# Kernel optimization log

Hardware: AMD Instinct MI355X
Metric: run time of the kernel (lower is better)

Reference implementation:

```python
import jax, jax.numpy as jnp
import numpy as np

N_NODES = 100000


def _sage_conv(x, edge_index, W_l, b_l, W_r):
    # PyG SAGEConv (aggr='mean', root_weight=True, normalize=False):
    # out = lin_l(mean_{j in N(i)} x_j) + lin_r(x_i)
    src, dst = edge_index[0], edge_index[1]
    n = x.shape[0]
    agg = jax.ops.segment_sum(x[src], dst, num_segments=n)
    cnt = jax.ops.segment_sum(jnp.ones((src.shape[0],), x.dtype), dst, num_segments=n)
    agg = agg / jnp.maximum(cnt, 1.0)[:, None]
    return agg @ W_l + b_l + x @ W_r


def setup_inputs() -> dict:
    key = jax.random.key(0)
    ks = jax.random.split(key, 12)
    in_dim, hidden = 384, 128
    x = jax.random.normal(ks[0], (N_NODES, in_dim), dtype=jnp.float32)
    edge_index = jax.random.randint(ks[1], (2, 3200000), 0, N_NODES, dtype=jnp.int32)
    pos_edge_label_index = jax.random.randint(ks[2], (2, 500000), 0, N_NODES, dtype=jnp.int32)
    neg_edge_label_index = jax.random.randint(ks[3], (2, 500000), 0, N_NODES, dtype=jnp.int32)
    s1 = 1.0 / np.sqrt(in_dim)
    s2 = 1.0 / np.sqrt(hidden)
    return {
        "x": x,
        "edge_index": edge_index,
        "pos_edge_label_index": pos_edge_label_index,
        "neg_edge_label_index": neg_edge_label_index,
        "W_l1": jax.random.uniform(ks[4], (in_dim, hidden), jnp.float32, -s1, s1),
        "b_l1": jnp.zeros((hidden,), jnp.float32),
        "W_r1": jax.random.uniform(ks[5], (in_dim, hidden), jnp.float32, -s1, s1),
        "W_l2": jax.random.uniform(ks[6], (hidden, hidden), jnp.float32, -s2, s2),
        "b_l2": jnp.zeros((hidden,), jnp.float32),
        "W_r2": jax.random.uniform(ks[7], (hidden, hidden), jnp.float32, -s2, s2),
        "W_lin": jax.random.uniform(ks[8], (2 * hidden, 1), jnp.float32, -s2, s2),
        "b_lin": jnp.zeros((1,), jnp.float32),
    }


def reference(x, edge_index, pos_edge_label_index, neg_edge_label_index,
              W_l1, b_l1, W_r1, W_l2, b_l2, W_r2, W_lin, b_lin):
    h = _sage_conv(x, edge_index, W_l1, b_l1, W_r1)
    h = jax.nn.relu(h)
    h = _sage_conv(h, edge_index, W_l2, b_l2, W_r2)

    def score(idx):
        pair = jnp.concatenate([h[idx[0]], h[idx[1]]], axis=1)  # [E, 2*hidden]
        return (pair @ W_lin + b_lin).reshape(-1)

    return score(pos_edge_label_index), score(neg_edge_label_index)
```

## Files before the change

### kernel.cpp

```cpp
#include <hip/hip_runtime.h>

#define IN_DIM 384
#define HID    128
#define NPB    256
#define BCAP   16384
#define LCAP   10240

#define AS1 __attribute__((address_space(1)))
#define AS3 __attribute__((address_space(3)))

typedef _Float16 half8 __attribute__((ext_vector_type(8)));
typedef _Float16 half2t __attribute__((ext_vector_type(2)));
typedef __fp16 fp16x2 __attribute__((ext_vector_type(2)));
typedef float floatx4 __attribute__((ext_vector_type(4)));

__global__ void zero_i32(int* __restrict__ p, int n) {
  int i = blockIdx.x * 256 + threadIdx.x;
  if (i < n) p[i] = 0;
}

__global__ __launch_bounds__(512) void partition_kernel(
    const int* __restrict__ src, const int* __restrict__ dst, int E, int nB,
    int* __restrict__ bCur, unsigned* __restrict__ bucketData) {
  __shared__ int hist[391];
  __shared__ int gbase[391];
  const int t = threadIdx.x;
  const int b0 = blockIdx.x * 8192;

  for (int i = t; i < nB; i += 512) hist[i] = 0;
  __syncthreads();
#pragma unroll
  for (int i = 0; i < 16; ++i) {
    int e = b0 + i * 512 + t;
    if (e < E) atomicAdd(&hist[dst[e] >> 8], 1);
  }
  __syncthreads();
  for (int i = t; i < nB; i += 512) {
    int h = hist[i];
    gbase[i] = h ? (i * BCAP + atomicAdd(&bCur[i], h)) : 0;
    hist[i] = 0;
  }
  __syncthreads();
#pragma unroll
  for (int i = 0; i < 16; ++i) {
    int e = b0 + i * 512 + t;
    if (e < E) {
      int d = dst[e];
      int b = d >> 8;
      int r = atomicAdd(&hist[b], 1);
      bucketData[gbase[b] + r] = ((unsigned)(d & 255) << 17) | (unsigned)src[e];
    }
  }
}

__global__ __launch_bounds__(1024) void node_sort3(
    const unsigned* __restrict__ bucketData, const int* __restrict__ bCur,
    int N, int* __restrict__ sorted_src, int* __restrict__ rs, int* __restrict__ re) {
  extern __shared__ unsigned sdata[];
  __shared__ int hist[NPB];
  __shared__ int s[NPB];
  __shared__ int cur[NPB];
  const int b = blockIdx.x;
  const int t = threadIdx.x;
  const int start = b * BCAP;
  const int fill = bCur[b];
  if (t < NPB) hist[t] = 0;
  __syncthreads();
  for (int i = t; i < fill; i += 1024) {
    unsigned d = bucketData[start + i];
    if (i < LCAP) sdata[i] = d;
    atomicAdd(&hist[d >> 17], 1);
  }
  __syncthreads();
  int v = 0;
  if (t < NPB) { v = hist[t]; s[t] = v; }
  __syncthreads();
  for (int off = 1; off < NPB; off <<= 1) {
    int y = (t < NPB && t >= off) ? s[t - off] : 0;
    __syncthreads();
    if (t < NPB) s[t] += y;
    __syncthreads();
  }
  if (t < NPB) {
    int excl = s[t] - v;
    const int node = b * NPB + t;
    if (node < N) {
      rs[node] = start + excl;
      re[node] = start + excl + v;
    }
    cur[t] = start + excl;
  }
  __syncthreads();
  for (int i = t; i < fill; i += 1024) {
    unsigned d = (i < LCAP) ? sdata[i] : bucketData[start + i];
    int p = atomicAdd(&cur[d >> 17], 1);
    sorted_src[p] = (int)(d & 0x1FFFF);
  }
}

__global__ void pack_w2(const float* __restrict__ Wl, const float* __restrict__ Wr,
                        _Float16* __restrict__ Bp) {
  const float* __restrict__ W = blockIdx.z ? Wr : Wl;
  const int tn = blockIdx.x;
  const int ks = blockIdx.y;
  const int KS = gridDim.y;
  const int lane = threadIdx.x;
  const int n = tn * 16 + (lane & 15);
  const int kb = ks * 32 + (lane >> 4) * 8;
  half8 v;
#pragma unroll
  for (int j = 0; j < 8; ++j) v[j] = (_Float16)W[(size_t)(kb + j) * HID + n];
  *(half8*)(Bp + (((size_t)(blockIdx.z * 8 + tn) * KS + ks) * 64 + lane) * 8) = v;
}

__device__ inline half2t cvt_pk(float a, float b) {
  fp16x2 r = __builtin_amdgcn_cvt_pkrtz(a, b);
  union { fp16x2 f; half2t h; } c;
  c.f = r;
  return c.h;
}

__global__ __launch_bounds__(512) void gemm_f32a(
    const float* __restrict__ A, int M,
    const _Float16* __restrict__ Bp, _Float16* __restrict__ C) {
  __shared__ float As[128 * 32];

  const int K = IN_DIM, KS = IN_DIM / 32;
  const int tid = threadIdx.x;
  const int lane = tid & 63;
  const int wid = tid >> 6;
  const int quad = lane >> 4;
  const int lm = lane & 15;
  const int row0 = (wid & 1) * 64;
  const int ct0 = (wid >> 1) * 4;
  const int blockRow = blockIdx.x * 128;

  const int srow = lane >> 3;
  const int scol = ((lane & 7) ^ (srow & 7)) * 4;
  const int grow0 = min(blockRow + wid * 16 + srow, M - 1);
  const int grow1 = min(blockRow + wid * 16 + 8 + srow, M - 1);

  floatx4 acc[16];
#pragma unroll
  for (int i = 0; i < 16; ++i) {
    acc[i][0] = 0.f; acc[i][1] = 0.f; acc[i][2] = 0.f; acc[i][3] = 0.f;
  }

  for (int ks = 0; ks < KS; ++ks) {
    const int k0 = ks * 32;
    __syncthreads();
    __builtin_amdgcn_global_load_lds(
        (const AS1 void*)(A + (size_t)grow0 * K + k0 + scol),
        (AS3 void*)(As + (wid * 16) * 32), 16, 0, 0);
    __builtin_amdgcn_global_load_lds(
        (const AS1 void*)(A + (size_t)grow1 * K + k0 + scol),
        (AS3 void*)(As + (wid * 16 + 8) * 32), 16, 0, 0);

    half8 bf[4];
#pragma unroll
    for (int ct = 0; ct < 4; ++ct)
      bf[ct] = *(const half8*)(Bp + (((size_t)(ct0 + ct) * KS + ks) * 64 + lane) * 8);

    __syncthreads();

    half8 af[4];
#pragma unroll
    for (int rt = 0; rt < 4; ++rt) {
      const int row = row0 + rt * 16 + lm;
      const int sw = row & 7;
      const floatx4 fA = *(const floatx4*)&As[(row * 8 + ((quad * 2) ^ sw)) * 4];
      const floatx4 fB = *(const floatx4*)&As[(row * 8 + ((quad * 2 + 1) ^ sw)) * 4];
      half2t h01 = cvt_pk(fA[0], fA[1]);
      half2t h23 = cvt_pk(fA[2], fA[3]);
      half2t h45 = cvt_pk(fB[0], fB[1]);
      half2t h67 = cvt_pk(fB[2], fB[3]);
      half8 a;
      a[0] = h01[0]; a[1] = h01[1]; a[2] = h23[0]; a[3] = h23[1];
      a[4] = h45[0]; a[5] = h45[1]; a[6] = h67[0]; a[7] = h67[1];
      af[rt] = a;
    }
#pragma unroll
    for (int rt = 0; rt < 4; ++rt)
#pragma unroll
      for (int ct = 0; ct < 4; ++ct)
        acc[rt * 4 + ct] =
            __builtin_amdgcn_mfma_f32_16x16x32_f16(af[rt], bf[ct], acc[rt * 4 + ct], 0, 0, 0);
  }

#pragma unroll
  for (int rt = 0; rt < 4; ++rt) {
#pragma unroll
    for (int r = 0; r < 4; ++r) {
      const int gm = blockRow + row0 + rt * 16 + quad * 4 + r;
      if (gm < M) {
#pragma unroll
        for (int ct = 0; ct < 4; ++ct)
          C[(size_t)gm * 256 + (ct0 + ct) * 16 + lm] = (_Float16)acc[rt * 4 + ct][r];
      }
    }
  }
}

__global__ __launch_bounds__(512) void gemm_f16a(
    const _Float16* __restrict__ A, int M,
    const _Float16* __restrict__ Bp, _Float16* __restrict__ C) {
  __shared__ _Float16 As[128 * 32];

  const int K = HID, KS = HID / 32;
  const int tid = threadIdx.x;
  const int lane = tid & 63;
  const int wid = tid >> 6;
  const int quad = lane >> 4;
  const int lm = lane & 15;
  const int row0 = (wid & 1) * 64;
  const int ct0 = (wid >> 1) * 4;
  const int blockRow = blockIdx.x * 128;

  const int srow = lane >> 2;
  const int scol = ((lane & 3) ^ ((lane >> 3) & 3)) * 8;
  const int grow = min(blockRow + wid * 16 + srow, M - 1);

  floatx4 acc[16];
#pragma unroll
  for (int i = 0; i < 16; ++i) {
    acc[i][0] = 0.f; acc[i][1] = 0.f; acc[i][2] = 0.f; acc[i][3] = 0.f;
  }

  for (int ks = 0; ks < KS; ++ks) {
    const int k0 = ks * 32;
    __syncthreads();
    __builtin_amdgcn_global_load_lds(
        (const AS1 void*)(A + (size_t)grow * K + k0 + scol),
        (AS3 void*)(As + (wid * 16) * 32), 16, 0, 0);

    half8 bf[4];
#pragma unroll
    for (int ct = 0; ct < 4; ++ct)
      bf[ct] = *(const half8*)(Bp + (((size_t)(ct0 + ct) * KS + ks) * 64 + lane) * 8);

    __syncthreads();

    half8 af[4];
#pragma unroll
    for (int rt = 0; rt < 4; ++rt) {
      const int row = row0 + rt * 16 + lm;
      const int cg = quad ^ ((row >> 1) & 3);
      af[rt] = *(const half8*)&As[(row * 4 + cg) * 8];
    }
#pragma unroll
    for (int rt = 0; rt < 4; ++rt)
#pragma unroll
      for (int ct = 0; ct < 4; ++ct)
        acc[rt * 4 + ct] =
            __builtin_amdgcn_mfma_f32_16x16x32_f16(af[rt], bf[ct], acc[rt * 4 + ct], 0, 0, 0);
  }

#pragma unroll
  for (int rt = 0; rt < 4; ++rt) {
#pragma unroll
    for (int r = 0; r < 4; ++r) {
      const int gm = blockRow + row0 + rt * 16 + quad * 4 + r;
      if (gm < M) {
#pragma unroll
        for (int ct = 0; ct < 4; ++ct)
          C[(size_t)gm * 256 + (ct0 + ct) * 16 + lm] = (_Float16)acc[rt * 4 + ct][r];
      }
    }
  }
}

__device__ inline float2 upk(unsigned u) {
  union { unsigned v; _Float16 h[2]; } c; c.v = u;
  return make_float2((float)c.h[0], (float)c.h[1]);
}
__device__ inline half2t as_h2(unsigned u) {
  union { unsigned v; half2t h; } c; c.v = u;
  return c.h;
}
__device__ inline unsigned as_u32(half2t h) {
  union { half2t h; unsigned v; } c; c.h = h;
  return c.v;
}
__device__ inline unsigned pkadd(unsigned a, unsigned b) {
  return as_u32(as_h2(a) + as_h2(b));
}
__device__ inline void pkacc4(uint4& A, const uint4& v) {
  A.x = pkadd(A.x, v.x); A.y = pkadd(A.y, v.y);
  A.z = pkadd(A.z, v.z); A.w = pkadd(A.w, v.w);
}

__device__ inline uint4 gather_rows(const unsigned* __restrict__ yzu,
                                    const int* __restrict__ sorted_src,
                                    int start, int end, int cl, int slot) {
  uint4 A0 = make_uint4(0u, 0u, 0u, 0u);
  uint4 A1 = A0;
  int k = start + slot;
  for (; k + 12 < end; k += 16) {
    int s0 = sorted_src[k];
    int s1 = sorted_src[k + 4];
    int s2 = sorted_src[k + 8];
    int s3 = sorted_src[k + 12];
    uint4 v0 = *(const uint4*)(yzu + (size_t)s0 * 128 + cl * 4);
    uint4 v1 = *(const uint4*)(yzu + (size_t)s1 * 128 + cl * 4);
    uint4 v2 = *(const uint4*)(yzu + (size_t)s2 * 128 + cl * 4);
    uint4 v3 = *(const uint4*)(yzu + (size_t)s3 * 128 + cl * 4);
    pkacc4(A0, v0);
    pkacc4(A1, v1);
    pkacc4(A0, v2);
    pkacc4(A1, v3);
  }
  if (k + 4 < end) {
    int s0 = sorted_src[k];
    int s1 = sorted_src[k + 4];
    uint4 v0 = *(const uint4*)(yzu + (size_t)s0 * 128 + cl * 4);
    uint4 v1 = *(const uint4*)(yzu + (size_t)s1 * 128 + cl * 4);
    pkacc4(A0, v0);
    pkacc4(A1, v1);
    k += 8;
  }
  if (k < end) {
    int s = sorted_src[k];
    uint4 v = *(const uint4*)(yzu + (size_t)s * 128 + cl * 4);
    pkacc4(A0, v);
  }
  pkacc4(A0, A1);
#pragma unroll
  for (int off = 16; off < 64; off <<= 1) {
    uint4 o;
    o.x = (unsigned)__shfl_xor((int)A0.x, off, 64);
    o.y = (unsigned)__shfl_xor((int)A0.y, off, 64);
    o.z = (unsigned)__shfl_xor((int)A0.z, off, 64);
    o.w = (unsigned)__shfl_xor((int)A0.w, off, 64);
    pkacc4(A0, o);
  }
  return A0;
}

__global__ __launch_bounds__(256) void agg_relu16(
    const unsigned* __restrict__ yzu, const int* __restrict__ sorted_src,
    const int* __restrict__ rs, const int* __restrict__ re,
    const float* __restrict__ bias, unsigned* __restrict__ h1u, int N) {
  const int w = threadIdx.x >> 6;
  const int lane = threadIdx.x & 63;
  const int cl = lane & 15;
  const int slot = lane >> 4;
  const int node = blockIdx.x * 4 + w;
  if (node >= N) return;
  const int start = rs[node];
  const int end = re[node];
  uint4 A = gather_rows(yzu, sorted_src, start, end, cl, slot);
  if (slot == 0) {
    const int deg = end - start;
    const float inv = 1.f / (float)max(deg, 1);
    uint4 z4 = *(const uint4*)(yzu + (size_t)node * 128 + 64 + cl * 4);
    const unsigned av[4] = {A.x, A.y, A.z, A.w};
    const unsigned zv[4] = {z4.x, z4.y, z4.z, z4.w};
    uint4 o;
    unsigned ov[4];
#pragma unroll
    for (int q = 0; q < 4; ++q) {
      const int cp = cl * 4 + q;
      float2 a = upk(av[q]);
      float2 z = upk(zv[q]);
      float vx = fmaxf(a.x * inv + bias[2 * cp] + z.x, 0.f);
      float vy = fmaxf(a.y * inv + bias[2 * cp + 1] + z.y, 0.f);
      union { unsigned v; _Float16 h[2]; } c;
      c.h[0] = (_Float16)vx; c.h[1] = (_Float16)vy;
      ov[q] = c.v;
    }
    o.x = ov[0]; o.y = ov[1]; o.z = ov[2]; o.w = ov[3];
    *(uint4*)(h1u + (size_t)node * 64 + cl * 4) = o;
  }
}

__global__ __launch_bounds__(256) void agg_score16(
    const unsigned* __restrict__ yzu, const int* __restrict__ sorted_src,
    const int* __restrict__ rs, const int* __restrict__ re,
    const float* __restrict__ bias, const float* __restrict__ Wlin,
    float* __restrict__ sa, float* __restrict__ sb, int N) {
  const int w = threadIdx.x >> 6;
  const int lane = threadIdx.x & 63;
  const int cl = lane & 15;
  const int slot = lane >> 4;
  const int node = blockIdx.x * 4 + w;
  if (node >= N) return;
  const int start = rs[node];
  const int end = re[node];
  uint4 A = gather_rows(yzu, sorted_src, start, end, cl, slot);
  const int deg = end - start;
  const float inv = 1.f / (float)max(deg, 1);
  uint4 z4 = *(const uint4*)(yzu + (size_t)node * 128 + 64 + cl * 4);
  const unsigned av[4] = {A.x, A.y, A.z, A.w};
  const unsigned zv[4] = {z4.x, z4.y, z4.z, z4.w};
  float pa = 0.f, pb = 0.f;
#pragma unroll
  for (int q = 0; q < 4; ++q) {
    const int cp = cl * 4 + q;
    float2 a = upk(av[q]);
    float2 z = upk(zv[q]);
    float hx = a.x * inv + bias[2 * cp] + z.x;
    float hy = a.y * inv + bias[2 * cp + 1] + z.y;
    pa += hx * Wlin[2 * cp] + hy * Wlin[2 * cp + 1];
    pb += hx * Wlin[128 + 2 * cp] + hy * Wlin[129 + 2 * cp];
  }
#pragma unroll
  for (int off = 1; off < 16; off <<= 1) {
    pa += __shfl_xor(pa, off, 64);
    pb += __shfl_xor(pb, off, 64);
  }
  if (lane == 0) {
    sa[node] = pa;
    sb[node] = pb;
  }
}

__global__ void score2(const int* __restrict__ pos, const int* __restrict__ neg,
                       int Ep, int En,
                       const float* __restrict__ sa, const float* __restrict__ sb,
                       const float* __restrict__ blin, float* __restrict__ out) {
  int e = blockIdx.x * 256 + threadIdx.x;
  if (e < Ep) {
    out[e] = sa[pos[e]] + sb[pos[Ep + e]] + blin[0];
  } else if (e < Ep + En) {
    int i = e - Ep;
    out[Ep + i] = sa[neg[i]] + sb[neg[En + i]] + blin[0];
  }
}

extern "C" void kernel_launch(void* const* d_in, const int* in_sizes, int n_in,
                              void* d_out, int out_size, void* d_ws, size_t ws_size,
                              hipStream_t stream) {
  (void)n_in; (void)out_size; (void)ws_size;
  const float* x    = (const float*)d_in[0];
  const int*   ei   = (const int*)d_in[1];
  const int*   pos  = (const int*)d_in[2];
  const int*   neg  = (const int*)d_in[3];
  const float* Wl1  = (const float*)d_in[4];
  const float* bl1  = (const float*)d_in[5];
  const float* Wr1  = (const float*)d_in[6];
  const float* Wl2  = (const float*)d_in[7];
  const float* bl2  = (const float*)d_in[8];
  const float* Wr2  = (const float*)d_in[9];
  const float* Wlin = (const float*)d_in[10];
  const float* blin = (const float*)d_in[11];

  const int N  = in_sizes[0] / IN_DIM;
  const int E  = in_sizes[1] / 2;
  const int Ep = in_sizes[2] / 2;
  const int En = in_sizes[3] / 2;
  const int* e_src = ei;
  const int* e_dst = ei + E;

  char* ws = (char*)d_ws;
  size_t off = 0;
  auto carve = [&](size_t bytes) -> char* {
    char* p = ws + off;
    off += (bytes + 255) & ~(size_t)255;
    return p;
  };
  const int nB = (N + NPB - 1) / NPB;
  const int KS1 = IN_DIM / 32;
  const int KS2 = HID / 32;

  int*      rs     = (int*)carve((size_t)N * 4);
  int*      re     = (int*)carve((size_t)N * 4);
  int*      bCur   = (int*)carve(512 * 4);
  unsigned* bData  = (unsigned*)carve((size_t)nB * BCAP * 4);
  int*      sorted = (int*)carve((size_t)nB * BCAP * 4);
  float*    sa     = (float*)carve((size_t)N * 4);
  float*    sb     = (float*)carve((size_t)N * 4);
  _Float16* Bp1    = (_Float16*)carve((size_t)16 * KS1 * 64 * 8 * 2);
  _Float16* Bp2    = (_Float16*)carve((size_t)16 * KS2 * 64 * 8 * 2);
  _Float16* yz     = (_Float16*)carve((size_t)N * 256 * 2);
  _Float16* h1     = (_Float16*)carve((size_t)N * 128 * 2);

  const int gemmBlocks = (N + 127) / 128;
  const int partBlocks = (E + 8191) / 8192;

  hipLaunchKernelGGL(zero_i32, dim3(2), dim3(256), 0, stream, bCur, 512);
  hipLaunchKernelGGL(partition_kernel, dim3(partBlocks), dim3(512), 0, stream,
                     e_src, e_dst, E, nB, bCur, bData);
  hipLaunchKernelGGL(node_sort3, dim3(nB), dim3(1024), LCAP * 4, stream,
                     bData, bCur, N, sorted, rs, re);

  hipLaunchKernelGGL(pack_w2, dim3(8, KS1, 2), dim3(64), 0, stream, Wl1, Wr1, Bp1);
  hipLaunchKernelGGL(pack_w2, dim3(8, KS2, 2), dim3(64), 0, stream, Wl2, Wr2, Bp2);

  hipLaunchKernelGGL(gemm_f32a, dim3(gemmBlocks), dim3(512), 0, stream,
                     x, N, Bp1, yz);
  hipLaunchKernelGGL(agg_relu16, dim3((N + 3) / 4), dim3(256), 0, stream,
                     (const unsigned*)yz, sorted, rs, re, bl1, (unsigned*)h1, N);
  hipLaunchKernelGGL(gemm_f16a, dim3(gemmBlocks), dim3(512), 0, stream,
                     h1, N, Bp2, yz);
  hipLaunchKernelGGL(agg_score16, dim3((N + 3) / 4), dim3(256), 0, stream,
                     (const unsigned*)yz, sorted, rs, re, bl2, Wlin, sa, sb, N);

  float* out = (float*)d_out;
  hipLaunchKernelGGL(score2, dim3((Ep + En + 255) / 256), dim3(256), 0, stream,
                     pos, neg, Ep, En, sa, sb, blin, out);
}
```

Before: 593.1 us.

## Split GEMM output into column-group planes and aggregate per group for cache locality

The GEMM outputs are now written in a column-group-major layout: eight planes of 16 half columns for the neighbour projection and eight for the root projection. The aggregation kernels launch eight times as many blocks, and each block gathers only its 32-byte slice per neighbour, so the table each block touches is small enough to stay cache-resident. The score kernel now accumulates partial dot products with float atomics, and the partition kernel zeroes the sa/sb buffers first. The cost is eight reads of each index list, many more atomics, strided GEMM stores, and 32-byte gathers that may use memory transactions poorly.

```diff
diff --git a/kernel.cpp b/kernel.cpp
--- a/kernel.cpp
+++ b/kernel.cpp
@@ -21,11 +21,14 @@
 
 __global__ __launch_bounds__(512) void partition_kernel(
     const int* __restrict__ src, const int* __restrict__ dst, int E, int nB,
-    int* __restrict__ bCur, unsigned* __restrict__ bucketData) {
+    int* __restrict__ bCur, unsigned* __restrict__ bucketData,
+    float* __restrict__ sab, int sabN) {
   __shared__ int hist[391];
   __shared__ int gbase[391];
   const int t = threadIdx.x;
   const int b0 = blockIdx.x * 8192;
+
+  for (int i = blockIdx.x * 512 + t; i < sabN; i += gridDim.x * 512) sab[i] = 0.f;
 
   for (int i = t; i < nB; i += 512) hist[i] = 0;
   __syncthreads();
@@ -119,6 +122,7 @@
   c.f = r;
   return c.h;
 }
+
 
 __global__ __launch_bounds__(512) void gemm_f32a(
     const float* __restrict__ A, int M,
@@ -194,8 +198,12 @@
       const int gm = blockRow + row0 + rt * 16 + quad * 4 + r;
       if (gm < M) {
 #pragma unroll
-        for (int ct = 0; ct < 4; ++ct)
-          C[(size_t)gm * 256 + (ct0 + ct) * 16 + lm] = (_Float16)acc[rt * 4 + ct][r];
+        for (int ct = 0; ct < 4; ++ct) {
+          const int tn = ct0 + ct;
+          _Float16* dst = C + ((size_t)(tn & 7) * M + gm) * 16 + lm;
+          if (tn >= 8) dst += (size_t)M * 128;
+          *dst = (_Float16)acc[rt * 4 + ct][r];
+        }
       }
     }
   }
@@ -262,8 +270,12 @@
       const int gm = blockRow + row0 + rt * 16 + quad * 4 + r;
       if (gm < M) {
 #pragma unroll
-        for (int ct = 0; ct < 4; ++ct)
-          C[(size_t)gm * 256 + (ct0 + ct) * 16 + lm] = (_Float16)acc[rt * 4 + ct][r];
+        for (int ct = 0; ct < 4; ++ct) {
+          const int tn = ct0 + ct;
+          _Float16* dst = C + ((size_t)(tn & 7) * M + gm) * 16 + lm;
+          if (tn >= 8) dst += (size_t)M * 128;
+          *dst = (_Float16)acc[rt * 4 + ct][r];
+        }
       }
     }
   }
@@ -284,133 +296,115 @@
 __device__ inline unsigned pkadd(unsigned a, unsigned b) {
   return as_u32(as_h2(a) + as_h2(b));
 }
-__device__ inline void pkacc4(uint4& A, const uint4& v) {
-  A.x = pkadd(A.x, v.x); A.y = pkadd(A.y, v.y);
-  A.z = pkadd(A.z, v.z); A.w = pkadd(A.w, v.w);
-}
-
-__device__ inline uint4 gather_rows(const unsigned* __restrict__ yzu,
-                                    const int* __restrict__ sorted_src,
-                                    int start, int end, int cl, int slot) {
-  uint4 A0 = make_uint4(0u, 0u, 0u, 0u);
-  uint4 A1 = A0;
+__device__ inline uint2 pkadd2(uint2 a, uint2 b) {
+  a.x = pkadd(a.x, b.x); a.y = pkadd(a.y, b.y); return a;
+}
+
+__device__ inline uint2 gather_group(const unsigned* __restrict__ yg,
+                                     const int* __restrict__ sorted_src,
+                                     int start, int end, int cl, int slot) {
+  uint2 A0 = make_uint2(0u, 0u);
+  uint2 A1 = make_uint2(0u, 0u);
   int k = start + slot;
-  for (; k + 12 < end; k += 16) {
+  for (; k + 16 < end; k += 32) {
     int s0 = sorted_src[k];
-    int s1 = sorted_src[k + 4];
-    int s2 = sorted_src[k + 8];
-    int s3 = sorted_src[k + 12];
-    uint4 v0 = *(const uint4*)(yzu + (size_t)s0 * 128 + cl * 4);
-    uint4 v1 = *(const uint4*)(yzu + (size_t)s1 * 128 + cl * 4);
-    uint4 v2 = *(const uint4*)(yzu + (size_t)s2 * 128 + cl * 4);
-    uint4 v3 = *(const uint4*)(yzu + (size_t)s3 * 128 + cl * 4);
-    pkacc4(A0, v0);
-    pkacc4(A1, v1);
-    pkacc4(A0, v2);
-    pkacc4(A1, v3);
-  }
-  if (k + 4 < end) {
-    int s0 = sorted_src[k];
-    int s1 = sorted_src[k + 4];
-    uint4 v0 = *(const uint4*)(yzu + (size_t)s0 * 128 + cl * 4);
-    uint4 v1 = *(const uint4*)(yzu + (size_t)s1 * 128 + cl * 4);
-    pkacc4(A0, v0);
-    pkacc4(A1, v1);
-    k += 8;
+    int s1 = sorted_src[k + 16];
+    uint2 v0 = *(const uint2*)(yg + (size_t)s0 * 8 + cl * 2);
+    uint2 v1 = *(const uint2*)(yg + (size_t)s1 * 8 + cl * 2);
+    A0 = pkadd2(A0, v0);
+    A1 = pkadd2(A1, v1);
   }
   if (k < end) {
-    int s = sorted_src[k];
-    uint4 v = *(const uint4*)(yzu + (size_t)s * 128 + cl * 4);
-    pkacc4(A0, v);
-  }
-  pkacc4(A0, A1);
-#pragma unroll
-  for (int off = 16; off < 64; off <<= 1) {
-    uint4 o;
+    uint2 v = *(const uint2*)(yg + (size_t)sorted_src[k] * 8 + cl * 2);
+    A0 = pkadd2(A0, v);
+  }
+  A0 = pkadd2(A0, A1);
+#pragma unroll
+  for (int off = 4; off < 64; off <<= 1) {
+    uint2 o;
     o.x = (unsigned)__shfl_xor((int)A0.x, off, 64);
     o.y = (unsigned)__shfl_xor((int)A0.y, off, 64);
-    o.z = (unsigned)__shfl_xor((int)A0.z, off, 64);
-    o.w = (unsigned)__shfl_xor((int)A0.w, off, 64);
-    pkacc4(A0, o);
+    A0 = pkadd2(A0, o);
   }
   return A0;
 }
 
-__global__ __launch_bounds__(256) void agg_relu16(
+__global__ __launch_bounds__(256) void agg_relu_split(
     const unsigned* __restrict__ yzu, const int* __restrict__ sorted_src,
     const int* __restrict__ rs, const int* __restrict__ re,
     const float* __restrict__ bias, unsigned* __restrict__ h1u, int N) {
+  const int g = blockIdx.x & 7;
+  const int nb = blockIdx.x >> 3;
   const int w = threadIdx.x >> 6;
   const int lane = threadIdx.x & 63;
-  const int cl = lane & 15;
-  const int slot = lane >> 4;
-  const int node = blockIdx.x * 4 + w;
+  const int cl = lane & 3;
+  const int slot = lane >> 2;
+  const int node = nb * 4 + w;
   if (node >= N) return;
   const int start = rs[node];
   const int end = re[node];
-  uint4 A = gather_rows(yzu, sorted_src, start, end, cl, slot);
+  const unsigned* __restrict__ yg = yzu + (size_t)g * N * 8;
+  uint2 A = gather_group(yg, sorted_src, start, end, cl, slot);
   if (slot == 0) {
     const int deg = end - start;
     const float inv = 1.f / (float)max(deg, 1);
-    uint4 z4 = *(const uint4*)(yzu + (size_t)node * 128 + 64 + cl * 4);
-    const unsigned av[4] = {A.x, A.y, A.z, A.w};
-    const unsigned zv[4] = {z4.x, z4.y, z4.z, z4.w};
-    uint4 o;
-    unsigned ov[4];
-#pragma unroll
-    for (int q = 0; q < 4; ++q) {
-      const int cp = cl * 4 + q;
-      float2 a = upk(av[q]);
-      float2 z = upk(zv[q]);
-      float vx = fmaxf(a.x * inv + bias[2 * cp] + z.x, 0.f);
-      float vy = fmaxf(a.y * inv + bias[2 * cp + 1] + z.y, 0.f);
-      union { unsigned v; _Float16 h[2]; } c;
-      c.h[0] = (_Float16)vx; c.h[1] = (_Float16)vy;
-      ov[q] = c.v;
-    }
-    o.x = ov[0]; o.y = ov[1]; o.z = ov[2]; o.w = ov[3];
-    *(uint4*)(h1u + (size_t)node * 64 + cl * 4) = o;
-  }
-}
-
-__global__ __launch_bounds__(256) void agg_score16(
+    uint2 z2 = *(const uint2*)(yzu + (size_t)N * 64 + ((size_t)g * N + node) * 8 + cl * 2);
+    float2 a0 = upk(A.x);
+    float2 a1 = upk(A.y);
+    float2 z0 = upk(z2.x);
+    float2 z1 = upk(z2.y);
+    const int c = g * 16 + cl * 4;
+    float v0 = fmaxf(a0.x * inv + bias[c]     + z0.x, 0.f);
+    float v1 = fmaxf(a0.y * inv + bias[c + 1] + z0.y, 0.f);
+    float v2 = fmaxf(a1.x * inv + bias[c + 2] + z1.x, 0.f);
+    float v3 = fmaxf(a1.y * inv + bias[c + 3] + z1.y, 0.f);
+    union { unsigned v; _Float16 h[2]; } cc;
+    uint2 o;
+    cc.h[0] = (_Float16)v0; cc.h[1] = (_Float16)v1; o.x = cc.v;
+    cc.h[0] = (_Float16)v2; cc.h[1] = (_Float16)v3; o.y = cc.v;
+    *(uint2*)(h1u + (size_t)node * 64 + g * 8 + cl * 2) = o;
+  }
+}
+
+__global__ __launch_bounds__(256) void agg_score_split(
     const unsigned* __restrict__ yzu, const int* __restrict__ sorted_src,
     const int* __restrict__ rs, const int* __restrict__ re,
     const float* __restrict__ bias, const float* __restrict__ Wlin,
     float* __restrict__ sa, float* __restrict__ sb, int N) {
+  const int g = blockIdx.x & 7;
+  const int nb = blockIdx.x >> 3;
   const int w = threadIdx.x >> 6;
   const int lane = threadIdx.x & 63;
-  const int cl = lane & 15;
-  const int slot = lane >> 4;
-  const int node = blockIdx.x * 4 + w;
+  const int cl = lane & 3;
+  const int slot = lane >> 2;
+  const int node = nb * 4 + w;
   if (node >= N) return;
   const int start = rs[node];
   const int end = re[node];
-  uint4 A = gather_rows(yzu, sorted_src, start, end, cl, slot);
-  const int deg = end - start;
-  const float inv = 1.f / (float)max(deg, 1);
-  uint4 z4 = *(const uint4*)(yzu + (size_t)node * 128 + 64 + cl * 4);
-  const unsigned av[4] = {A.x, A.y, A.z, A.w};
-  const unsigned zv[4] = {z4.x, z4.y, z4.z, z4.w};
-  float pa = 0.f, pb = 0.f;
-#pragma unroll
-  for (int q = 0; q < 4; ++q) {
-    const int cp = cl * 4 + q;
-    float2 a = upk(av[q]);
-    float2 z = upk(zv[q]);
-    float hx = a.x * inv + bias[2 * cp] + z.x;
-    float hy = a.y * inv + bias[2 * cp + 1] + z.y;
-    pa += hx * Wlin[2 * cp] + hy * Wlin[2 * cp + 1];
-    pb += hx * Wlin[128 + 2 * cp] + hy * Wlin[129 + 2 * cp];
-  }
-#pragma unroll
-  for (int off = 1; off < 16; off <<= 1) {
-    pa += __shfl_xor(pa, off, 64);
-    pb += __shfl_xor(pb, off, 64);
-  }
-  if (lane == 0) {
-    sa[node] = pa;
-    sb[node] = pb;
+  const unsigned* __restrict__ yg = yzu + (size_t)g * N * 8;
+  uint2 A = gather_group(yg, sorted_src, start, end, cl, slot);
+  if (slot == 0) {
+    const int deg = end - start;
+    const float inv = 1.f / (float)max(deg, 1);
+    uint2 z2 = *(const uint2*)(yzu + (size_t)N * 64 + ((size_t)g * N + node) * 8 + cl * 2);
+    float2 a0 = upk(A.x);
+    float2 a1 = upk(A.y);
+    float2 z0 = upk(z2.x);
+    float2 z1 = upk(z2.y);
+    const int c = g * 16 + cl * 4;
+    float h0 = a0.x * inv + bias[c]     + z0.x;
+    float h1 = a0.y * inv + bias[c + 1] + z0.y;
+    float h2 = a1.x * inv + bias[c + 2] + z1.x;
+    float h3 = a1.y * inv + bias[c + 3] + z1.y;
+    float pa = h0 * Wlin[c] + h1 * Wlin[c + 1] + h2 * Wlin[c + 2] + h3 * Wlin[c + 3];
+    float pb = h0 * Wlin[128 + c] + h1 * Wlin[129 + c] +
+               h2 * Wlin[130 + c] + h3 * Wlin[131 + c];
+    pa += __shfl_xor(pa, 1, 64); pb += __shfl_xor(pb, 1, 64);
+    pa += __shfl_xor(pa, 2, 64); pb += __shfl_xor(pb, 2, 64);
+    if (cl == 0) {
+      atomicAdd(&sa[node], pa);
+      atomicAdd(&sb[node], pb);
+    }
   }
 }
 
@@ -467,19 +461,22 @@
   int*      bCur   = (int*)carve(512 * 4);
   unsigned* bData  = (unsigned*)carve((size_t)nB * BCAP * 4);
   int*      sorted = (int*)carve((size_t)nB * BCAP * 4);
-  float*    sa     = (float*)carve((size_t)N * 4);
-  float*    sb     = (float*)carve((size_t)N * 4);
+  float*    sab    = (float*)carve((size_t)2 * N * 4);
   _Float16* Bp1    = (_Float16*)carve((size_t)16 * KS1 * 64 * 8 * 2);
   _Float16* Bp2    = (_Float16*)carve((size_t)16 * KS2 * 64 * 8 * 2);
   _Float16* yz     = (_Float16*)carve((size_t)N * 256 * 2);
   _Float16* h1     = (_Float16*)carve((size_t)N * 128 * 2);
 
+  float* sa = sab;
+  float* sb = sab + N;
+
   const int gemmBlocks = (N + 127) / 128;
   const int partBlocks = (E + 8191) / 8192;
+  const int aggBlocks  = ((N + 3) / 4) * 8;
 
   hipLaunchKernelGGL(zero_i32, dim3(2), dim3(256), 0, stream, bCur, 512);
   hipLaunchKernelGGL(partition_kernel, dim3(partBlocks), dim3(512), 0, stream,
-                     e_src, e_dst, E, nB, bCur, bData);
+                     e_src, e_dst, E, nB, bCur, bData, sab, 2 * N);
   hipLaunchKernelGGL(node_sort3, dim3(nB), dim3(1024), LCAP * 4, stream,
                      bData, bCur, N, sorted, rs, re);
 
@@ -488,11 +485,11 @@
 
   hipLaunchKernelGGL(gemm_f32a, dim3(gemmBlocks), dim3(512), 0, stream,
                      x, N, Bp1, yz);
-  hipLaunchKernelGGL(agg_relu16, dim3((N + 3) / 4), dim3(256), 0, stream,
+  hipLaunchKernelGGL(agg_relu_split, dim3(aggBlocks), dim3(256), 0, stream,
                      (const unsigned*)yz, sorted, rs, re, bl1, (unsigned*)h1, N);
   hipLaunchKernelGGL(gemm_f16a, dim3(gemmBlocks), dim3(512), 0, stream,
                      h1, N, Bp2, yz);
-  hipLaunchKernelGGL(agg_score16, dim3((N + 3) / 4), dim3(256), 0, stream,
+  hipLaunchKernelGGL(agg_score_split, dim3(aggBlocks), dim3(256), 0, stream,
                      (const unsigned*)yz, sorted, rs, re, bl2, Wlin, sa, sb, N);
 
   float* out = (float*)d_out;
```

New measurement: 977.5 us. 1.65x slower.

## Replace two-pass bucket sort with global-atomic counting sort for CSR build

Applied to the files above, without the earlier changes.

Replaces the bucketed partition plus per-bucket LDS sort with a plain counting sort. It runs a global atomic histogram over destinations, a three-kernel exclusive scan over nodes, and a scatter using per-node global atomics. This removes the intermediate bucket buffer and its fixed per-bucket capacity. In exchange it relies on 3.2M global atomics, issued twice, with little locality, and adds several kernel launches. Neighbour order inside each segment becomes nondeterministic.

```diff
diff --git a/kernel.cpp b/kernel.cpp
--- a/kernel.cpp
+++ b/kernel.cpp
@@ -2,9 +2,6 @@
 
 #define IN_DIM 384
 #define HID    128
-#define NPB    256
-#define BCAP   16384
-#define LCAP   10240
 
 #define AS1 __attribute__((address_space(1)))
 #define AS3 __attribute__((address_space(3)))
@@ -19,82 +16,64 @@
   if (i < n) p[i] = 0;
 }
 
-__global__ __launch_bounds__(512) void partition_kernel(
-    const int* __restrict__ src, const int* __restrict__ dst, int E, int nB,
-    int* __restrict__ bCur, unsigned* __restrict__ bucketData) {
-  __shared__ int hist[391];
-  __shared__ int gbase[391];
+__global__ __launch_bounds__(256) void hist_kernel(
+    const int* __restrict__ dst, int E, int* __restrict__ cnt) {
+  for (int i = blockIdx.x * 256 + threadIdx.x; i < E; i += gridDim.x * 256)
+    atomicAdd(&cnt[dst[i]], 1);
+}
+
+__global__ __launch_bounds__(256) void scan_block(
+    const int* __restrict__ cnt, int N, int* __restrict__ rs, int* __restrict__ bsum) {
+  __shared__ int s[256];
   const int t = threadIdx.x;
-  const int b0 = blockIdx.x * 8192;
-
-  for (int i = t; i < nB; i += 512) hist[i] = 0;
+  const int node = blockIdx.x * 256 + t;
+  int v = (node < N) ? cnt[node] : 0;
+  s[t] = v;
   __syncthreads();
-#pragma unroll
-  for (int i = 0; i < 16; ++i) {
-    int e = b0 + i * 512 + t;
-    if (e < E) atomicAdd(&hist[dst[e] >> 8], 1);
-  }
+  for (int off = 1; off < 256; off <<= 1) {
+    int y = (t >= off) ? s[t - off] : 0;
+    __syncthreads();
+    s[t] += y;
+    __syncthreads();
+  }
+  if (node < N) rs[node] = s[t] - v;
+  if (t == 255) bsum[blockIdx.x] = s[255];
+}
+
+__global__ __launch_bounds__(512) void scan_top(int* __restrict__ bsum, int nBlk) {
+  __shared__ int s[512];
+  const int t = threadIdx.x;
+  int v = (t < nBlk) ? bsum[t] : 0;
+  s[t] = v;
   __syncthreads();
-  for (int i = t; i < nB; i += 512) {
-    int h = hist[i];
-    gbase[i] = h ? (i * BCAP + atomicAdd(&bCur[i], h)) : 0;
-    hist[i] = 0;
-  }
-  __syncthreads();
-#pragma unroll
-  for (int i = 0; i < 16; ++i) {
-    int e = b0 + i * 512 + t;
-    if (e < E) {
-      int d = dst[e];
-      int b = d >> 8;
-      int r = atomicAdd(&hist[b], 1);
-      bucketData[gbase[b] + r] = ((unsigned)(d & 255) << 17) | (unsigned)src[e];
-    }
-  }
-}
-
-__global__ __launch_bounds__(1024) void node_sort3(
-    const unsigned* __restrict__ bucketData, const int* __restrict__ bCur,
-    int N, int* __restrict__ sorted_src, int* __restrict__ rs, int* __restrict__ re) {
-  extern __shared__ unsigned sdata[];
-  __shared__ int hist[NPB];
-  __shared__ int s[NPB];
-  __shared__ int cur[NPB];
-  const int b = blockIdx.x;
-  const int t = threadIdx.x;
-  const int start = b * BCAP;
-  const int fill = bCur[b];
-  if (t < NPB) hist[t] = 0;
-  __syncthreads();
-  for (int i = t; i < fill; i += 1024) {
-    unsigned d = bucketData[start + i];
-    if (i < LCAP) sdata[i] = d;
-    atomicAdd(&hist[d >> 17], 1);
-  }
-  __syncthreads();
-  int v = 0;
-  if (t < NPB) { v = hist[t]; s[t] = v; }
-  __syncthreads();
-  for (int off = 1; off < NPB; off <<= 1) {
-    int y = (t < NPB && t >= off) ? s[t - off] : 0;
-    __syncthreads();
-    if (t < NPB) s[t] += y;
-    __syncthreads();
-  }
-  if (t < NPB) {
-    int excl = s[t] - v;
-    const int node = b * NPB + t;
-    if (node < N) {
-      rs[node] = start + excl;
-      re[node] = start + excl + v;
-    }
-    cur[t] = start + excl;
-  }
-  __syncthreads();
-  for (int i = t; i < fill; i += 1024) {
-    unsigned d = (i < LCAP) ? sdata[i] : bucketData[start + i];
-    int p = atomicAdd(&cur[d >> 17], 1);
-    sorted_src[p] = (int)(d & 0x1FFFF);
+  for (int off = 1; off < 512; off <<= 1) {
+    int y = (t >= off) ? s[t - off] : 0;
+    __syncthreads();
+    s[t] += y;
+    __syncthreads();
+  }
+  if (t < nBlk) bsum[t] = s[t] - v;
+}
+
+__global__ __launch_bounds__(256) void scan_add(
+    const int* __restrict__ cnt, const int* __restrict__ bsum, int N,
+    int* __restrict__ rs, int* __restrict__ re, int* __restrict__ cur) {
+  const int node = blockIdx.x * 256 + threadIdx.x;
+  if (node < N) {
+    int r = rs[node] + bsum[blockIdx.x];
+    rs[node] = r;
+    cur[node] = r;
+    re[node] = r + cnt[node];
+  }
+}
+
+__global__ __launch_bounds__(256) void scatter_kernel(
+    const int* __restrict__ src, const int* __restrict__ dst, int E,
+    int* __restrict__ cur, int* __restrict__ sorted_src) {
+  for (int i = blockIdx.x * 256 + threadIdx.x; i < E; i += gridDim.x * 256) {
+    int d = dst[i];
+    int p = atomicAdd(&cur[d], 1);
+    sorted_src[p] = src[i];
   }
 }
 
@@ -458,15 +437,16 @@
     off += (bytes + 255) & ~(size_t)255;
     return p;
   };
-  const int nB = (N + NPB - 1) / NPB;
   const int KS1 = IN_DIM / 32;
   const int KS2 = HID / 32;
+  const int scanBlocks = (N + 255) / 256;
 
   int*      rs     = (int*)carve((size_t)N * 4);
   int*      re     = (int*)carve((size_t)N * 4);
-  int*      bCur   = (int*)carve(512 * 4);
-  unsigned* bData  = (unsigned*)carve((size_t)nB * BCAP * 4);
-  int*      sorted = (int*)carve((size_t)nB * BCAP * 4);
+  int*      cnt    = (int*)carve((size_t)N * 4);
+  int*      cur    = (int*)carve((size_t)N * 4);
+  int*      bsum   = (int*)carve(512 * 4);
+  int*      sorted = (int*)carve((size_t)E * 4);
   float*    sa     = (float*)carve((size_t)N * 4);
   float*    sb     = (float*)carve((size_t)N * 4);
   _Float16* Bp1    = (_Float16*)carve((size_t)16 * KS1 * 64 * 8 * 2);
@@ -475,13 +455,16 @@
   _Float16* h1     = (_Float16*)carve((size_t)N * 128 * 2);
 
   const int gemmBlocks = (N + 127) / 128;
-  const int partBlocks = (E + 8191) / 8192;
-
-  hipLaunchKernelGGL(zero_i32, dim3(2), dim3(256), 0, stream, bCur, 512);
-  hipLaunchKernelGGL(partition_kernel, dim3(partBlocks), dim3(512), 0, stream,
-                     e_src, e_dst, E, nB, bCur, bData);
-  hipLaunchKernelGGL(node_sort3, dim3(nB), dim3(1024), LCAP * 4, stream,
-                     bData, bCur, N, sorted, rs, re);
+
+  hipLaunchKernelGGL(zero_i32, dim3(scanBlocks), dim3(256), 0, stream, cnt, N);
+  hipLaunchKernelGGL(hist_kernel, dim3(2048), dim3(256), 0, stream, e_dst, E, cnt);
+  hipLaunchKernelGGL(scan_block, dim3(scanBlocks), dim3(256), 0, stream,
+                     cnt, N, rs, bsum);
+  hipLaunchKernelGGL(scan_top, dim3(1), dim3(512), 0, stream, bsum, scanBlocks);
+  hipLaunchKernelGGL(scan_add, dim3(scanBlocks), dim3(256), 0, stream,
+                     cnt, bsum, N, rs, re, cur);
+  hipLaunchKernelGGL(scatter_kernel, dim3(2048), dim3(256), 0, stream,
+                     e_src, e_dst, E, cur, sorted);
 
   hipLaunchKernelGGL(pack_w2, dim3(8, KS1, 2), dim3(64), 0, stream, Wl1, Wr1, Bp1);
   hipLaunchKernelGGL(pack_w2, dim3(8, KS2, 2), dim3(64), 0, stream, Wl2, Wr2, Bp2);
```

New measurement: 911.4 us. +53.7%, slower.
